# Optimization experiments

Measured on AMD Instinct MI355X. Metric: run time of the kernel, lower is better.

Reference implementation:

```python
import jax, jax.numpy as jnp
import numpy as np
import math

E = 8          # num_experts (= max_expert_num)
M = 1024       # hidden_size
H = 4096       # expert FFN dim (4*hidden)
B, S = 4, 4096 # batch, seq
CAP_FACTOR = 1.0
MIN_CAPACITY = 4


def setup_inputs() -> dict:
    key = jax.random.key(0)
    ks = jax.random.split(key, 5)
    hidden_states = jax.random.normal(ks[0], (B, S, M), dtype=jnp.float32)
    wg = jax.random.normal(ks[1], (M, E), dtype=jnp.float32) * (M ** -0.5)  # gate Linear (no bias, as in TopKGate)
    w1 = jax.random.normal(ks[2], (E, M, H), dtype=jnp.float32) * (M ** -0.5)
    b1 = jnp.zeros((E, H), dtype=jnp.float32)
    w2 = jax.random.normal(ks[3], (E, H, M), dtype=jnp.float32) * (H ** -0.5)
    b2 = jnp.zeros((E, M), dtype=jnp.float32)
    return {"hidden_states": hidden_states, "wg": wg, "w1": w1, "b1": b1, "w2": w2, "b2": b2}


def reference(hidden_states, wg, w1, b1, w2, b2):
    b, s_len, m = hidden_states.shape
    x = hidden_states.reshape(-1, m)            # [s, m], s = tokens
    s = x.shape[0]
    capacity = max(int(math.ceil(s / E * CAP_FACTOR)), MIN_CAPACITY)  # static

    # ---- top-1 gating (DeepSpeed top1gating, fp32, no jitter, no RTS) ----
    logits = x.astype(jnp.float32) @ wg          # [s, e]
    gates = jax.nn.softmax(logits, axis=1)
    idx = jnp.argmax(gates, axis=1)              # chosen expert per token
    mask1 = jax.nn.one_hot(idx, E, dtype=jnp.float32)
    exp_counts = jnp.sum(mask1, axis=0).astype(jnp.int32)
    ce = jnp.mean(mask1, axis=0)                 # fraction routed per expert (pre-drop)
    me = jnp.mean(gates, axis=0)
    l_aux = jnp.sum(me * ce) * E                 # load-balancing loss

    # position of each token within its expert's queue; drop past capacity
    locations = jnp.cumsum(mask1, axis=0) - 1.0  # [s, e]
    loc = jnp.sum(locations * mask1, axis=1).astype(jnp.int32)  # [s]
    keep = (loc < capacity).astype(jnp.float32)  # capacity drop mask
    gate_s = jnp.sum(gates * mask1, axis=1) * keep
    loc_c = jnp.clip(loc, 0, capacity - 1)

    # ---- dispatch: scatter tokens to [E, C, M] slots (equiv. to einsum('sec,sm->ecm')) ----
    dispatched = jnp.zeros((E, capacity, m), dtype=x.dtype).at[idx, loc_c].add(x * keep[:, None])

    # ---- grouped expert GEMMs (MLP with GELU) ----
    h = jax.nn.gelu(jnp.einsum('ecm,emh->ech', dispatched, w1) + b1[:, None, :])
    eout = jnp.einsum('ech,ehm->ecm', h, w2) + b2[:, None, :]

    # ---- combine: gather back and scale by gate value (dropped tokens -> 0) ----
    out = eout[idx, loc_c] * gate_s[:, None]     # [s, m]
    return out.reshape(b, s_len, m), l_aux, exp_counts
```

## Files before the change

kernel.cpp:

```cpp
#include <hip/hip_runtime.h>
#include <hip/hip_bf16.h>

#define TOKENS 16384
#define MDIM   1024
#define HDIM   4096
#define NEXP   8
#define EGRP   4
#define CAP    2048

typedef __attribute__((ext_vector_type(8))) short bf16x8;
typedef __attribute__((ext_vector_type(4))) float f32x4;

__device__ __forceinline__ short f2bf(float x) {
  unsigned u = __float_as_uint(x);
  unsigned r = (u + 0x7fffu + ((u >> 16) & 1u)) >> 16;
  return (short)r;
}

__device__ __forceinline__ float gelu_f(float x) {
  float u = 1.5957691216057308f * (x + 0.044715f * x * x * x);
  float e = __expf(u);
  return x * (1.f - 1.f / (e + 1.f));
}

__global__ __launch_bounds__(256) void gating_kernel(
    const float* __restrict__ x, const float* __restrict__ wg,
    int* __restrict__ idx, float* __restrict__ gate,
    float* __restrict__ mepart, short* __restrict__ xb) {
  __shared__ float me_s[NEXP];
  int tid = threadIdx.x, wid = tid >> 6, lane = tid & 63;
  if (tid < NEXP) me_s[tid] = 0.f;
  __syncthreads();
  int t = blockIdx.x * 4 + wid;
  float acc[NEXP];
#pragma unroll
  for (int e = 0; e < NEXP; e++) acc[e] = 0.f;
  const float4* xr = (const float4*)(x + (size_t)t * MDIM);
  short* xbr = xb + (size_t)t * MDIM + lane * 16;
#pragma unroll
  for (int j = 0; j < 4; j++) {
    float4 xv = xr[lane * 4 + j];
    short4 bv; bv.x = f2bf(xv.x); bv.y = f2bf(xv.y); bv.z = f2bf(xv.z); bv.w = f2bf(xv.w);
    ((short4*)(xbr))[j] = bv;
    int base = lane * 16 + j * 4;
    const float* xp = &xv.x;
#pragma unroll
    for (int i = 0; i < 4; i++) {
      float xi = xp[i];
      const float4* wr = (const float4*)(wg + (size_t)(base + i) * NEXP);
      float4 w0 = wr[0], w1 = wr[1];
      acc[0] += xi * w0.x; acc[1] += xi * w0.y; acc[2] += xi * w0.z; acc[3] += xi * w0.w;
      acc[4] += xi * w1.x; acc[5] += xi * w1.y; acc[6] += xi * w1.z; acc[7] += xi * w1.w;
    }
  }
#pragma unroll
  for (int off = 32; off > 0; off >>= 1)
#pragma unroll
    for (int e = 0; e < NEXP; e++) acc[e] += __shfl_xor(acc[e], off, 64);
  if (lane == 0) {
    float mx = acc[0]; int ai = 0;
#pragma unroll
    for (int e = 1; e < NEXP; e++) if (acc[e] > mx) { mx = acc[e]; ai = e; }
    float ex[NEXP]; float se = 0.f;
#pragma unroll
    for (int e = 0; e < NEXP; e++) { ex[e] = __expf(acc[e] - mx); se += ex[e]; }
    float inv = 1.f / se;
#pragma unroll
    for (int e = 0; e < NEXP; e++) atomicAdd(&me_s[e], ex[e] * inv);
    idx[t] = ai;
    gate[t] = inv;
  }
  __syncthreads();
  if (tid < NEXP) mepart[blockIdx.x * NEXP + tid] = me_s[tid];
}

__global__ __launch_bounds__(1024) void scan_kernel(
    const int* __restrict__ idx, float* __restrict__ gate,
    int* __restrict__ s2t, int* __restrict__ counts) {
  __shared__ int wcnt[16][NEXP];
  __shared__ int base[NEXP];
  int tid = threadIdx.x, wid = tid >> 6, lane = tid & 63;
  if (tid < NEXP) base[tid] = 0;
  __syncthreads();
  for (int chunk = 0; chunk < TOKENS; chunk += 1024) {
    int i = chunk + tid;
    int e = idx[i];
    int pre = 0;
#pragma unroll
    for (int e2 = 0; e2 < NEXP; e2++) {
      unsigned long long b = __ballot(e == e2);
      if (e2 == e) pre = __popcll(b & ((1ull << lane) - 1ull));
      if (lane == 0) wcnt[wid][e2] = __popcll(b);
    }
    __syncthreads();
    int off = base[e];
    for (int w = 0; w < wid; w++) off += wcnt[w][e];
    int loc = off + pre;
    if (loc < CAP) s2t[e * CAP + loc] = i;
    else           gate[i] = 0.f;
    __syncthreads();
    if (tid < NEXP) {
      int tsum = 0;
#pragma unroll
      for (int w = 0; w < 16; w++) tsum += wcnt[w][tid];
      base[tid] += tsum;
    }
    __syncthreads();
  }
  if (tid < NEXP) counts[tid] = base[tid];
}

__global__ __launch_bounds__(256) void finalize_kernel(
    const float* __restrict__ mepart, const int* __restrict__ counts,
    float* __restrict__ out_tail, int nblocks) {
  __shared__ float red[256];
  __shared__ float me[NEXP];
  int tid = threadIdx.x;
  float s = 0.f;
  int e = tid & 7;
  for (int r = tid >> 3; r < nblocks; r += 32) s += mepart[r * NEXP + e];
  red[tid] = s;
  __syncthreads();
  if (tid < NEXP) {
    float tsum = 0.f;
    for (int i = tid; i < 256; i += 8) tsum += red[i];
    me[tid] = tsum;
  }
  __syncthreads();
  if (tid == 0) {
    float la = 0.f;
    for (int k = 0; k < NEXP; k++)
      la += (me[k] / (float)TOKENS) * ((float)counts[k] / (float)TOKENS);
    out_tail[0] = la * (float)NEXP;
  }
  if (tid < NEXP) out_tail[1 + tid] = (float)counts[tid];
}

__global__ __launch_bounds__(256) void transpose_cvt_kernel(
    const float* __restrict__ in, short* __restrict__ out, int R, int Cc) {
  __shared__ float tile[32][33];
  int e = blockIdx.z;
  const float* in_e = in + (size_t)e * R * Cc;
  short* out_e = out + (size_t)e * R * Cc;
  int r0 = blockIdx.y * 32, c0 = blockIdx.x * 32;
  int tx = threadIdx.x & 31, ty = threadIdx.x >> 5;
#pragma unroll
  for (int i = 0; i < 4; i++)
    tile[ty + i * 8][tx] = in_e[(size_t)(r0 + ty + i * 8) * Cc + c0 + tx];
  __syncthreads();
#pragma unroll
  for (int i = 0; i < 4; i++)
    out_e[(size_t)(c0 + ty + i * 8) * R + r0 + tx] = f2bf(tile[tx][ty + i * 8]);
}

__device__ __forceinline__ void stage_tile(const short* __restrict__ g0, int ldk,
                                           short* lds, int tid) {
  int w = tid >> 6, lane = tid & 63;
#pragma unroll
  for (int i = 0; i < 4; i++) {
    int rbase = w * 32 + i * 8;
    int r = rbase + (lane >> 3);
    int c = (lane & 7) ^ (r & 7);
    const short* g = g0 + (size_t)r * ldk + c * 8;
    short* l = lds + rbase * 64;
    __builtin_amdgcn_global_load_lds((const __attribute__((address_space(1))) void*)g,
                                     (__attribute__((address_space(3))) void*)l,
                                     16, 0, 0);
  }
}

__global__ __launch_bounds__(256) void gemm1_kernel(
    const short* __restrict__ xb, const int* __restrict__ s2t,
    const short* __restrict__ W1t, const float* __restrict__ b1,
    short* __restrict__ Hh, const short* __restrict__ zrow, int eg) {
  __shared__ __align__(16) short ldsA[128 * 64];
  __shared__ __align__(16) short ldsB[128 * 64];
  int bz = blockIdx.z, bm = blockIdx.y, bn = blockIdx.x;
  int e_abs = eg + bz;
  const short* Be = W1t + ((size_t)e_abs * HDIM + (size_t)bn * 128) * MDIM;
  int tid = threadIdx.x, lane = tid & 63, w = tid >> 6;
  const short* aptr[4];
#pragma unroll
  for (int i = 0; i < 4; i++) {
    int rb = w * 32 + i * 8;
    int r = rb + (lane >> 3);
    int tok = s2t[e_abs * CAP + bm * 128 + r];
    const short* basep = (tok >= 0) ? (xb + (size_t)tok * MDIM) : zrow;
    aptr[i] = basep + (((lane & 7) ^ (r & 7)) * 8);
  }
  int wr = (w >> 1) * 64, wc = (w & 1) * 64;
  f32x4 acc[4][4];
  f32x4 zero = {0.f, 0.f, 0.f, 0.f};
#pragma unroll
  for (int a = 0; a < 4; a++)
#pragma unroll
    for (int b = 0; b < 4; b++) acc[a][b] = zero;
  for (int kt = 0; kt < MDIM; kt += 64) {
    __syncthreads();
#pragma unroll
    for (int i = 0; i < 4; i++) {
      short* l = ldsA + (w * 32 + i * 8) * 64;
      __builtin_amdgcn_global_load_lds((const __attribute__((address_space(1))) void*)(aptr[i] + kt),
                                       (__attribute__((address_space(3))) void*)l,
                                       16, 0, 0);
    }
    stage_tile(Be + kt, MDIM, ldsB, tid);
    __syncthreads();
#pragma unroll
    for (int kk = 0; kk < 2; kk++) {
      bf16x8 af[4], bfr[4];
#pragma unroll
      for (int rt = 0; rt < 4; rt++) {
        int r = wr + rt * 16 + (lane & 15);
        int c = (kk * 4 + (lane >> 4)) ^ (r & 7);
        af[rt] = *(const bf16x8*)(ldsA + r * 64 + c * 8);
      }
#pragma unroll
      for (int ct = 0; ct < 4; ct++) {
        int r = wc + ct * 16 + (lane & 15);
        int c = (kk * 4 + (lane >> 4)) ^ (r & 7);
        bfr[ct] = *(const bf16x8*)(ldsB + r * 64 + c * 8);
      }
#pragma unroll
      for (int rt = 0; rt < 4; rt++)
#pragma unroll
        for (int ct = 0; ct < 4; ct++)
          acc[rt][ct] = __builtin_amdgcn_mfma_f32_16x16x32_bf16(af[rt], bfr[ct], acc[rt][ct], 0, 0, 0);
    }
  }
  int q = lane >> 4, ln = lane & 15;
#pragma unroll
  for (int ct = 0; ct < 4; ct++) {
    int col = bn * 128 + wc + ct * 16 + ln;
    float bias = b1[e_abs * HDIM + col];
#pragma unroll
    for (int rt = 0; rt < 4; rt++) {
#pragma unroll
      for (int rg = 0; rg < 4; rg++) {
        int row = bm * 128 + wr + rt * 16 + q * 4 + rg;
        float v = acc[rt][ct][rg] + bias;
        Hh[((size_t)bz * CAP + row) * HDIM + col] = f2bf(gelu_f(v));
      }
    }
  }
}

__global__ __launch_bounds__(256) void gemm2_kernel(
    const short* __restrict__ Hh, const short* __restrict__ W2t,
    const float* __restrict__ b2, const int* __restrict__ s2t,
    const float* __restrict__ gate, float* __restrict__ out, int eg) {
  __shared__ __align__(16) short ldsA[128 * 64];
  __shared__ __align__(16) short ldsB[128 * 64];
  int bz = blockIdx.z, bm = blockIdx.y, bn = blockIdx.x;
  int e_abs = eg + bz;
  const short* Ae = Hh + ((size_t)bz * CAP + (size_t)bm * 128) * HDIM;
  const short* Be = W2t + ((size_t)e_abs * MDIM + (size_t)bn * 128) * HDIM;
  int tid = threadIdx.x, lane = tid & 63, w = tid >> 6;
  int wr = (w >> 1) * 64, wc = (w & 1) * 64;
  f32x4 acc[4][4];
  f32x4 zero = {0.f, 0.f, 0.f, 0.f};
#pragma unroll
  for (int a = 0; a < 4; a++)
#pragma unroll
    for (int b = 0; b < 4; b++) acc[a][b] = zero;
  for (int kt = 0; kt < HDIM; kt += 64) {
    __syncthreads();
    stage_tile(Ae + kt, HDIM, ldsA, tid);
    stage_tile(Be + kt, HDIM, ldsB, tid);
    __syncthreads();
#pragma unroll
    for (int kk = 0; kk < 2; kk++) {
      bf16x8 af[4], bfr[4];
#pragma unroll
      for (int rt = 0; rt < 4; rt++) {
        int r = wr + rt * 16 + (lane & 15);
        int c = (kk * 4 + (lane >> 4)) ^ (r & 7);
        af[rt] = *(const bf16x8*)(ldsA + r * 64 + c * 8);
      }
#pragma unroll
      for (int ct = 0; ct < 4; ct++) {
        int r = wc + ct * 16 + (lane & 15);
        int c = (kk * 4 + (lane >> 4)) ^ (r & 7);
        bfr[ct] = *(const bf16x8*)(ldsB + r * 64 + c * 8);
      }
#pragma unroll
      for (int rt = 0; rt < 4; rt++)
#pragma unroll
        for (int ct = 0; ct < 4; ct++)
          acc[rt][ct] = __builtin_amdgcn_mfma_f32_16x16x32_bf16(af[rt], bfr[ct], acc[rt][ct], 0, 0, 0);
    }
  }
  int q = lane >> 4, ln = lane & 15;
  float bias[4];
#pragma unroll
  for (int ct = 0; ct < 4; ct++) bias[ct] = b2[e_abs * MDIM + bn * 128 + wc + ct * 16 + ln];
#pragma unroll
  for (int rt = 0; rt < 4; rt++) {
#pragma unroll
    for (int rg = 0; rg < 4; rg++) {
      int row = bm * 128 + wr + rt * 16 + q * 4 + rg;
      int token = s2t[e_abs * CAP + row];
      if (token < 0) continue;
      float g = gate[token];
#pragma unroll
      for (int ct = 0; ct < 4; ct++) {
        int col = bn * 128 + wc + ct * 16 + ln;
        out[(size_t)token * MDIM + col] = (acc[rt][ct][rg] + bias[ct]) * g;
      }
    }
  }
}

__global__ __launch_bounds__(256) void zerodrop_kernel(
    const float* __restrict__ gate, float* __restrict__ out) {
  int t = blockIdx.x;
  if (gate[t] != 0.f) return;
  float4 z = {0.f, 0.f, 0.f, 0.f};
  ((float4*)(out + (size_t)t * MDIM))[threadIdx.x] = z;
}

extern "C" void kernel_launch(void* const* d_in, const int* in_sizes, int n_in,
                              void* d_out, int out_size, void* d_ws, size_t ws_size,
                              hipStream_t stream) {
  const float* x  = (const float*)d_in[0];
  const float* wg = (const float*)d_in[1];
  const float* w1 = (const float*)d_in[2];
  const float* b1 = (const float*)d_in[3];
  const float* w2 = (const float*)d_in[4];
  const float* b2 = (const float*)d_in[5];
  float* out = (float*)d_out;

  char* ws = (char*)d_ws;
  size_t off = 0;
  auto alloc = [&](size_t n) { char* ptr = ws + off; off += (n + 255) & ~(size_t)255; return ptr; };
  short* W1t  = (short*)alloc((size_t)NEXP * MDIM * HDIM * 2);
  short* W2t  = (short*)alloc((size_t)NEXP * MDIM * HDIM * 2);
  short* Hh   = (short*)alloc((size_t)EGRP * CAP * HDIM * 2);
  short* xb   = (short*)alloc((size_t)TOKENS * MDIM * 2);
  short* zrow = (short*)alloc((size_t)MDIM * 2);
  int*   idx  = (int*)  alloc(TOKENS * 4);
  float* gate = (float*)alloc(TOKENS * 4);
  int*   s2t  = (int*)  alloc(NEXP * CAP * 4);
  float* mep  = (float*)alloc((TOKENS / 4) * NEXP * 4);
  int*   cnts = (int*)  alloc(NEXP * 4);
  if (ws_size < off) return;

  hipMemsetAsync(s2t, 0xFF, NEXP * CAP * 4, stream);
  hipMemsetAsync(zrow, 0, MDIM * 2, stream);

  gating_kernel<<<TOKENS / 4, 256, 0, stream>>>(x, wg, idx, gate, mep, xb);
  scan_kernel<<<1, 1024, 0, stream>>>(idx, gate, s2t, cnts);
  finalize_kernel<<<1, 256, 0, stream>>>(mep, cnts, out + (size_t)TOKENS * MDIM, TOKENS / 4);
  transpose_cvt_kernel<<<dim3(HDIM / 32, MDIM / 32, NEXP), 256, 0, stream>>>(w1, W1t, MDIM, HDIM);
  transpose_cvt_kernel<<<dim3(MDIM / 32, HDIM / 32, NEXP), 256, 0, stream>>>(w2, W2t, HDIM, MDIM);
  for (int g = 0; g < 2; g++) {
    gemm1_kernel<<<dim3(HDIM / 128, CAP / 128, EGRP), 256, 0, stream>>>(xb, s2t, W1t, b1, Hh, zrow, g * EGRP);
    gemm2_kernel<<<dim3(MDIM / 128, CAP / 128, EGRP), 256, 0, stream>>>(Hh, W2t, b2, s2t, gate, out, g * EGRP);
  }
  zerodrop_kernel<<<TOKENS, 256, 0, stream>>>(gate, out);
}
```

Baseline: 933.6 us.

## Vectorize GEMM epilogues, widen transpose tiles, and parallelize the routing scan

The MFMA operands are swapped so each lane holds four consecutive output columns. The GEMM1 GELU epilogue then writes packed bf16x4 and the GEMM2 scatter writes float4 rows with one token lookup per row, replacing scalar strided stores. The weight transpose-convert kernel now uses 64x64 tiles with float4 loads, a bf16 shared-memory tile and short4 stores. The single-block scan drops its per-chunk barriers: each wave counts 1024 tokens locally and a single cross-wave prefix follows. Together these aim to cut store transactions and launch-phase overhead, at the cost of more register pressure from the per-thread arrays in the scan.

```diff
diff --git a/kernel.cpp b/kernel.cpp
--- a/kernel.cpp
+++ b/kernel.cpp
@@ -15,6 +15,11 @@
   unsigned u = __float_as_uint(x);
   unsigned r = (u + 0x7fffu + ((u >> 16) & 1u)) >> 16;
   return (short)r;
+}
+
+__device__ __forceinline__ unsigned bfbits(float x) {
+  unsigned u = __float_as_uint(x);
+  return u + 0x7fffu + ((u >> 16) & 1u);
 }
 
 __device__ __forceinline__ float gelu_f(float x) {
@@ -78,36 +83,50 @@
     const int* __restrict__ idx, float* __restrict__ gate,
     int* __restrict__ s2t, int* __restrict__ counts) {
   __shared__ int wcnt[16][NEXP];
-  __shared__ int base[NEXP];
+  __shared__ int wbase[16][NEXP];
   int tid = threadIdx.x, wid = tid >> 6, lane = tid & 63;
-  if (tid < NEXP) base[tid] = 0;
-  __syncthreads();
-  for (int chunk = 0; chunk < TOKENS; chunk += 1024) {
-    int i = chunk + tid;
-    int e = idx[i];
-    int pre = 0;
+  unsigned long long ltmask = (1ull << lane) - 1ull;
+  int myexp[16], myloc[16];
+  int cnt[NEXP];
+#pragma unroll
+  for (int e = 0; e < NEXP; e++) cnt[e] = 0;
+  int base_tok = wid * 1024;
+#pragma unroll
+  for (int p = 0; p < 16; p++) {
+    int e = idx[base_tok + p * 64 + lane];
+    myexp[p] = e;
+    int pos = 0;
 #pragma unroll
     for (int e2 = 0; e2 < NEXP; e2++) {
       unsigned long long b = __ballot(e == e2);
-      if (e2 == e) pre = __popcll(b & ((1ull << lane) - 1ull));
-      if (lane == 0) wcnt[wid][e2] = __popcll(b);
-    }
-    __syncthreads();
-    int off = base[e];
-    for (int w = 0; w < wid; w++) off += wcnt[w][e];
-    int loc = off + pre;
+      if (e == e2) pos = cnt[e2] + __popcll(b & ltmask);
+      cnt[e2] += __popcll(b);
+    }
+    myloc[p] = pos;
+  }
+  if (lane < NEXP) wcnt[wid][lane] = cnt[lane];
+  __syncthreads();
+  if (tid < 128) {
+    int w = tid >> 3, e = tid & 7;
+    int s = 0;
+    for (int w2 = 0; w2 < w; w2++) s += wcnt[w2][e];
+    wbase[w][e] = s;
+  }
+  __syncthreads();
+#pragma unroll
+  for (int p = 0; p < 16; p++) {
+    int i = base_tok + p * 64 + lane;
+    int e = myexp[p];
+    int loc = wbase[wid][e] + myloc[p];
     if (loc < CAP) s2t[e * CAP + loc] = i;
     else           gate[i] = 0.f;
-    __syncthreads();
-    if (tid < NEXP) {
-      int tsum = 0;
-#pragma unroll
-      for (int w = 0; w < 16; w++) tsum += wcnt[w][tid];
-      base[tid] += tsum;
-    }
-    __syncthreads();
-  }
-  if (tid < NEXP) counts[tid] = base[tid];
+  }
+  if (tid < NEXP) {
+    int tot = 0;
+#pragma unroll
+    for (int w = 0; w < 16; w++) tot += wcnt[w][tid];
+    counts[tid] = tot;
+  }
 }
 
 __global__ __launch_bounds__(256) void finalize_kernel(
@@ -138,19 +157,35 @@
 
 __global__ __launch_bounds__(256) void transpose_cvt_kernel(
     const float* __restrict__ in, short* __restrict__ out, int R, int Cc) {
-  __shared__ float tile[32][33];
+  __shared__ short tile[64][72];
   int e = blockIdx.z;
   const float* in_e = in + (size_t)e * R * Cc;
   short* out_e = out + (size_t)e * R * Cc;
-  int r0 = blockIdx.y * 32, c0 = blockIdx.x * 32;
-  int tx = threadIdx.x & 31, ty = threadIdx.x >> 5;
-#pragma unroll
-  for (int i = 0; i < 4; i++)
-    tile[ty + i * 8][tx] = in_e[(size_t)(r0 + ty + i * 8) * Cc + c0 + tx];
-  __syncthreads();
-#pragma unroll
-  for (int i = 0; i < 4; i++)
-    out_e[(size_t)(c0 + ty + i * 8) * R + r0 + tx] = f2bf(tile[tx][ty + i * 8]);
+  int r0 = blockIdx.y * 64, c0 = blockIdx.x * 64;
+  int tid = threadIdx.x;
+#pragma unroll
+  for (int i = 0; i < 4; i++) {
+    int linear = tid + 256 * i;
+    int r = linear >> 4;
+    int f4 = linear & 15;
+    float4 v = *(const float4*)(in_e + (size_t)(r0 + r) * Cc + c0 + f4 * 4);
+    int c = f4 * 4;
+    tile[c + 0][r] = f2bf(v.x);
+    tile[c + 1][r] = f2bf(v.y);
+    tile[c + 2][r] = f2bf(v.z);
+    tile[c + 3][r] = f2bf(v.w);
+  }
+  __syncthreads();
+#pragma unroll
+  for (int i = 0; i < 4; i++) {
+    int linear = tid + 256 * i;
+    int c = linear >> 4;
+    int s4 = linear & 15;
+    short4 s;
+    s.x = tile[c][s4 * 4 + 0]; s.y = tile[c][s4 * 4 + 1];
+    s.z = tile[c][s4 * 4 + 2]; s.w = tile[c][s4 * 4 + 3];
+    *(short4*)(out_e + (size_t)(c0 + c) * R + r0 + s4 * 4) = s;
+  }
 }
 
 __device__ __forceinline__ void stage_tile(const short* __restrict__ g0, int ldk,
@@ -225,22 +260,26 @@
       for (int rt = 0; rt < 4; rt++)
 #pragma unroll
         for (int ct = 0; ct < 4; ct++)
-          acc[rt][ct] = __builtin_amdgcn_mfma_f32_16x16x32_bf16(af[rt], bfr[ct], acc[rt][ct], 0, 0, 0);
+          acc[ct][rt] = __builtin_amdgcn_mfma_f32_16x16x32_bf16(bfr[ct], af[rt], acc[ct][rt], 0, 0, 0);
     }
   }
   int q = lane >> 4, ln = lane & 15;
 #pragma unroll
-  for (int ct = 0; ct < 4; ct++) {
-    int col = bn * 128 + wc + ct * 16 + ln;
-    float bias = b1[e_abs * HDIM + col];
-#pragma unroll
-    for (int rt = 0; rt < 4; rt++) {
-#pragma unroll
-      for (int rg = 0; rg < 4; rg++) {
-        int row = bm * 128 + wr + rt * 16 + q * 4 + rg;
-        float v = acc[rt][ct][rg] + bias;
-        Hh[((size_t)bz * CAP + row) * HDIM + col] = f2bf(gelu_f(v));
-      }
+  for (int rt = 0; rt < 4; rt++) {
+    int caprow = bm * 128 + wr + rt * 16 + ln;
+    size_t rowoff = ((size_t)bz * CAP + caprow) * HDIM;
+#pragma unroll
+    for (int ct = 0; ct < 4; ct++) {
+      int colb = bn * 128 + wc + ct * 16 + q * 4;
+      float4 bias = *(const float4*)(b1 + (size_t)e_abs * HDIM + colb);
+      unsigned u0 = bfbits(gelu_f(acc[ct][rt][0] + bias.x));
+      unsigned u1 = bfbits(gelu_f(acc[ct][rt][1] + bias.y));
+      unsigned u2 = bfbits(gelu_f(acc[ct][rt][2] + bias.z));
+      unsigned u3 = bfbits(gelu_f(acc[ct][rt][3] + bias.w));
+      uint2 pk;
+      pk.x = __builtin_amdgcn_perm(u1, u0, 0x07060302u);
+      pk.y = __builtin_amdgcn_perm(u3, u2, 0x07060302u);
+      *(uint2*)(Hh + rowoff + colb) = pk;
     }
   }
 }
@@ -287,26 +326,27 @@
       for (int rt = 0; rt < 4; rt++)
 #pragma unroll
         for (int ct = 0; ct < 4; ct++)
-          acc[rt][ct] = __builtin_amdgcn_mfma_f32_16x16x32_bf16(af[rt], bfr[ct], acc[rt][ct], 0, 0, 0);
+          acc[ct][rt] = __builtin_amdgcn_mfma_f32_16x16x32_bf16(bfr[ct], af[rt], acc[ct][rt], 0, 0, 0);
     }
   }
   int q = lane >> 4, ln = lane & 15;
-  float bias[4];
-#pragma unroll
-  for (int ct = 0; ct < 4; ct++) bias[ct] = b2[e_abs * MDIM + bn * 128 + wc + ct * 16 + ln];
 #pragma unroll
   for (int rt = 0; rt < 4; rt++) {
-#pragma unroll
-    for (int rg = 0; rg < 4; rg++) {
-      int row = bm * 128 + wr + rt * 16 + q * 4 + rg;
-      int token = s2t[e_abs * CAP + row];
-      if (token < 0) continue;
-      float g = gate[token];
-#pragma unroll
-      for (int ct = 0; ct < 4; ct++) {
-        int col = bn * 128 + wc + ct * 16 + ln;
-        out[(size_t)token * MDIM + col] = (acc[rt][ct][rg] + bias[ct]) * g;
-      }
+    int caprow = bm * 128 + wr + rt * 16 + ln;
+    int token = s2t[e_abs * CAP + caprow];
+    if (token < 0) continue;
+    float g = gate[token];
+    float* orow = out + (size_t)token * MDIM;
+#pragma unroll
+    for (int ct = 0; ct < 4; ct++) {
+      int colb = bn * 128 + wc + ct * 16 + q * 4;
+      float4 bias = *(const float4*)(b2 + (size_t)e_abs * MDIM + colb);
+      float4 v;
+      v.x = (acc[ct][rt][0] + bias.x) * g;
+      v.y = (acc[ct][rt][1] + bias.y) * g;
+      v.z = (acc[ct][rt][2] + bias.z) * g;
+      v.w = (acc[ct][rt][3] + bias.w) * g;
+      *(float4*)(orow + colb) = v;
     }
   }
 }
@@ -351,8 +391,8 @@
   gating_kernel<<<TOKENS / 4, 256, 0, stream>>>(x, wg, idx, gate, mep, xb);
   scan_kernel<<<1, 1024, 0, stream>>>(idx, gate, s2t, cnts);
   finalize_kernel<<<1, 256, 0, stream>>>(mep, cnts, out + (size_t)TOKENS * MDIM, TOKENS / 4);
-  transpose_cvt_kernel<<<dim3(HDIM / 32, MDIM / 32, NEXP), 256, 0, stream>>>(w1, W1t, MDIM, HDIM);
-  transpose_cvt_kernel<<<dim3(MDIM / 32, HDIM / 32, NEXP), 256, 0, stream>>>(w2, W2t, HDIM, MDIM);
+  transpose_cvt_kernel<<<dim3(HDIM / 64, MDIM / 64, NEXP), 256, 0, stream>>>(w1, W1t, MDIM, HDIM);
+  transpose_cvt_kernel<<<dim3(MDIM / 64, HDIM / 64, NEXP), 256, 0, stream>>>(w2, W2t, HDIM, MDIM);
   for (int g = 0; g < 2; g++) {
     gemm1_kernel<<<dim3(HDIM / 128, CAP / 128, EGRP), 256, 0, stream>>>(xb, s2t, W1t, b1, Hh, zrow, g * EGRP);
     gemm2_kernel<<<dim3(MDIM / 128, CAP / 128, EGRP), 256, 0, stream>>>(Hh, W2t, b2, s2t, gate, out, g * EGRP);
```

Measured after the change: 915.6 us. Within noise of the previous version (-1.9%).
